# Optimization experiments

Hardware: AMD Instinct MI355X
Metric: run time of the kernel (lower is better)

## Reference

```python
import jax, jax.numpy as jnp
import numpy as np


def setup_inputs() -> dict:
    key = jax.random.key(0)
    k0, k1, k2 = jax.random.split(key, 3)
    B, S, E, U = 32, 2048, 512, 512
    return {
        "seq": jax.random.normal(k0, (B, S, E), jnp.float32),
        "w1": jax.random.normal(k1, (U, E), jnp.float32) * 0.05,
        "b1": jnp.zeros((U,), jnp.float32),
        "w2": jax.random.normal(k2, (3, U), jnp.float32) * 0.05,
        "b2": jnp.zeros((3,), jnp.float32),
        "num_lists": 16,
        "list_size": 16,
    }


def reference(seq, w1, b1, w2, b2, num_lists, list_size):
    B, S, E = seq.shape
    # action decoder: Linear -> SiLU -> Linear -> Softmax over 3 actions
    h = jax.nn.silu(jnp.einsum('bse,ue->bsu', seq, w1) + b1)
    actions = jax.nn.softmax(jnp.einsum('bsu,au->bsa', h, w2) + b2, axis=-1)  # (B,S,3)

    Hn, Wn = num_lists, list_size
    T0 = jnp.zeros((B, Hn, Wn), seq.dtype).at[:, 0, -1].set(1.0)   # superposition grid
    rs0 = jnp.zeros((B, Hn), seq.dtype).at[:, 0].set(1.0)          # row sums

    # process actions in reverse token order; scan over seq dim
    acts_rev = jnp.swapaxes(actions[:, ::-1, :], 0, 1)  # (S,B,3)

    def step(carry, a):
        T, rs = carry
        a0, a1, a2 = a[:, 0:1], a[:, 1:2], a[:, 2:3]  # each (B,1)
        # weight used to place the current (reversed) token: (a0+a1)*T
        w_step = (a0 + a1)[:, :, None] * T  # (B,H,W)
        # devolve: the grouped conv2d with kernel [0, a2, a0] is a width-shift blend
        other = a2[:, :, None] * T[:, :, :-1] + a0[:, :, None] * T[:, :, 1:]  # cols 0..W-2
        sums = a1 * jnp.roll(rs, 1, axis=1).at[:, 0].set(0.0)                 # (B,H)
        last = sums + a2 * T[:, :, -1]                                        # (B,H)
        rs_new = (a0 + a2) * rs + sums
        T_new = jnp.concatenate([other, last[:, :, None]], axis=2)
        return (T_new, rs_new), w_step

    _, ws = jax.lax.scan(step, (T0, rs0), acts_rev)  # ws: (S,B,H,W), aligned with reversed seq
    # G = sum_i w_i[...,None] * token_i[:,None,None,:]
    G = jnp.einsum('sbhw,bse->bhwe', ws, seq[:, ::-1, :])
    return G
```

## Files before the change

kernel.cpp:

```cpp
#include <hip/hip_runtime.h>
#include <stdint.h>

#define S_LEN 2048
#define NB 32
#define NE 512
#define NU 512
#define NP 256

typedef __bf16 bf16;
typedef __bf16 bf16x8 __attribute__((ext_vector_type(8)));
typedef __bf16 bf16x4 __attribute__((ext_vector_type(4)));
typedef float f32x4 __attribute__((ext_vector_type(4)));
typedef float f32x8 __attribute__((ext_vector_type(8)));

__device__ __forceinline__ void gload16(const void* g, void* l) {
    __builtin_amdgcn_global_load_lds(
        (__attribute__((address_space(1))) void*)g,
        (__attribute__((address_space(3))) void*)l, 16, 0, 0);
}

__device__ __forceinline__ float dpp_shr1_z(float x) {
    return __builtin_bit_cast(float, __builtin_amdgcn_update_dpp(
        0, __builtin_bit_cast(int, x), 0x111, 0xF, 0xF, true));
}
__device__ __forceinline__ float dpp_shl1_z(float x) {
    return __builtin_bit_cast(float, __builtin_amdgcn_update_dpp(
        0, __builtin_bit_cast(int, x), 0x101, 0xF, 0xF, true));
}

__device__ __forceinline__ void stage_tile(const bf16* __restrict__ src, int SR,
                                           bf16* lds, int tid) {
#pragma unroll
    for (int rnd = 0; rnd < 2; ++rnd) {
        const int c = rnd * 256 + tid;
        const int row = c >> 2;
        const int q = (c & 3) ^ ((c >> 3) & 3);
        gload16(src + (size_t)row * SR + q * 8, lds + c * 8);
    }
}

__global__ __launch_bounds__(256) void k_wconv(
    const float* __restrict__ w1, bf16* __restrict__ wHi, bf16* __restrict__ wLo)
{
    const int i = (blockIdx.x * 256 + threadIdx.x) * 4;
    const float4 v = *(const float4*)(w1 + i);
    const float vv[4] = {v.x, v.y, v.z, v.w};
    bf16x4 oh, ol;
#pragma unroll
    for (int q = 0; q < 4; ++q) {
        const bf16 hb = (bf16)vv[q];
        oh[q] = hb;
        ol[q] = (bf16)(vv[q] - (float)hb);
    }
    *(bf16x4*)(wHi + i) = oh;
    *(bf16x4*)(wLo + i) = ol;
}

__global__ __launch_bounds__(256, 2) void k_gemm1(
    const float* __restrict__ seq,
    const bf16* __restrict__ w1H, const bf16* __restrict__ w1L,
    const float* __restrict__ b1v, const float* __restrict__ w2,
    const float* __restrict__ b2v, float* __restrict__ actions)
{
    __shared__ __align__(16) bf16 BhL[2][4096];
    __shared__ __align__(16) bf16 BlL[2][4096];
    const int tid = threadIdx.x;
    const int wid = tid >> 6;
    const int lane = tid & 63;
    const int lr = lane & 15, lg = lane >> 4;
    const int m0 = blockIdx.x << 7;

    const float* arow0 = seq + (size_t)(m0 + wid * 32 + lr) * NE + lg * 8;
    const float* arow1 = arow0 + 16 * NE;
    const int lroff = lr * 64 + (lg ^ ((lr >> 1) & 3)) * 16;

    float plog[3][2][4];
#pragma unroll
    for (int a = 0; a < 3; ++a)
#pragma unroll
        for (int i = 0; i < 2; ++i)
#pragma unroll
            for (int q = 0; q < 4; ++q) plog[a][i][q] = 0.f;

    f32x4 acc[2][8];
    stage_tile(w1H, NE, BhL[0], tid);
    stage_tile(w1L, NE, BlL[0], tid);
    f32x8 Aa0 = *(const f32x8*)(arow0);
    f32x8 Aa1 = *(const f32x8*)(arow1);
    f32x8 Ab0, Ab1;

#define G1_BODY(g, buf, Ac0, Ac1, An0, An1) do {                              \
        __syncthreads();                                                      \
        if (((g) & 15) == 0) {                                                \
            _Pragma("unroll") for (int i = 0; i < 2; ++i)                     \
            _Pragma("unroll") for (int j = 0; j < 8; ++j)                     \
                acc[i][j] = (f32x4)(0.f);                                     \
        }                                                                     \
        bf16x8 bh[8], bl[8];                                                  \
        _Pragma("unroll") for (int j = 0; j < 8; ++j) {                       \
            bh[j] = *(const bf16x8*)((const char*)BhL[buf] + j * 1024 + lroff);\
            bl[j] = *(const bf16x8*)((const char*)BlL[buf] + j * 1024 + lroff);\
        }                                                                     \
        __syncthreads();                                                      \
        if ((g) < 63) {                                                       \
            const int gn = (g) + 1;                                           \
            const int u0n = (gn >> 4) << 7;                                   \
            const int k0n = (gn & 15) << 5;                                   \
            stage_tile(w1H + (size_t)u0n * NE + k0n, NE, BhL[(buf) ^ 1], tid);\
            stage_tile(w1L + (size_t)u0n * NE + k0n, NE, BlL[(buf) ^ 1], tid);\
            An0 = *(const f32x8*)(arow0 + k0n);                               \
            An1 = *(const f32x8*)(arow1 + k0n);                               \
        }                                                                     \
        bf16x8 Ah0, Al0, Ah1, Al1;                                            \
        _Pragma("unroll") for (int q = 0; q < 8; ++q) {                       \
            const bf16 h0 = (bf16)Ac0[q];                                     \
            Ah0[q] = h0; Al0[q] = (bf16)(Ac0[q] - (float)h0);                 \
            const bf16 h1 = (bf16)Ac1[q];                                     \
            Ah1[q] = h1; Al1[q] = (bf16)(Ac1[q] - (float)h1);                 \
        }                                                                     \
        _Pragma("unroll") for (int j = 0; j < 8; ++j) {                       \
            acc[0][j] = __builtin_amdgcn_mfma_f32_16x16x32_bf16(Ah0, bh[j], acc[0][j], 0, 0, 0); \
            acc[0][j] = __builtin_amdgcn_mfma_f32_16x16x32_bf16(Ah0, bl[j], acc[0][j], 0, 0, 0); \
            acc[0][j] = __builtin_amdgcn_mfma_f32_16x16x32_bf16(Al0, bh[j], acc[0][j], 0, 0, 0); \
            acc[1][j] = __builtin_amdgcn_mfma_f32_16x16x32_bf16(Ah1, bh[j], acc[1][j], 0, 0, 0); \
            acc[1][j] = __builtin_amdgcn_mfma_f32_16x16x32_bf16(Ah1, bl[j], acc[1][j], 0, 0, 0); \
            acc[1][j] = __builtin_amdgcn_mfma_f32_16x16x32_bf16(Al1, bh[j], acc[1][j], 0, 0, 0); \
        }                                                                     \
        if (((g) & 15) == 15) {                                               \
            const int u0 = ((g) >> 4) << 7;                                   \
            _Pragma("unroll") for (int j = 0; j < 8; ++j) {                   \
                const int col = u0 + j * 16 + lr;                             \
                const float b1c = b1v[col];                                   \
                const float w20 = w2[col], w21 = w2[NU + col], w22 = w2[2 * NU + col]; \
                _Pragma("unroll") for (int i = 0; i < 2; ++i)                 \
                _Pragma("unroll") for (int q = 0; q < 4; ++q) {               \
                    const float x = acc[i][j][q] + b1c;                       \
                    const float hgate = x / (1.f + __expf(-x));               \
                    plog[0][i][q] = fmaf(hgate, w20, plog[0][i][q]);          \
                    plog[1][i][q] = fmaf(hgate, w21, plog[1][i][q]);          \
                    plog[2][i][q] = fmaf(hgate, w22, plog[2][i][q]);          \
                }                                                             \
            }                                                                 \
        }                                                                     \
    } while (0)

    for (int gg = 0; gg < 32; ++gg) {
        G1_BODY(2 * gg, 0, Aa0, Aa1, Ab0, Ab1);
        G1_BODY(2 * gg + 1, 1, Ab0, Ab1, Aa0, Aa1);
    }
#undef G1_BODY

#pragma unroll
    for (int m = 1; m < 16; m <<= 1) {
#pragma unroll
        for (int a = 0; a < 3; ++a)
#pragma unroll
            for (int i = 0; i < 2; ++i)
#pragma unroll
                for (int q = 0; q < 4; ++q)
                    plog[a][i][q] += __shfl_xor(plog[a][i][q], m);
    }
    const float bb0 = b2v[0], bb1 = b2v[1], bb2 = b2v[2];
    if (lr == 0) {
#pragma unroll
        for (int i = 0; i < 2; ++i)
#pragma unroll
            for (int q = 0; q < 4; ++q) {
                const int row = m0 + wid * 32 + i * 16 + lg * 4 + q;
                const float l0 = plog[0][i][q] + bb0;
                const float l1 = plog[1][i][q] + bb1;
                const float l2 = plog[2][i][q] + bb2;
                const float mx = fmaxf(l0, fmaxf(l1, l2));
                const float e0 = __expf(l0 - mx), e1 = __expf(l1 - mx), e2 = __expf(l2 - mx);
                const float inv = 1.f / (e0 + e1 + e2);
                *(float4*)(actions + (size_t)row * 4) = make_float4(e0 * inv, e1 * inv, e2 * inv, 0.f);
            }
    }
}

union SPMem {
    float tile[64][65];
    struct {
        float4 actbuf[3][256];
        float  sums[2][256][16];
    } s;
};

__device__ __forceinline__ void rs_chunk(const float4* __restrict__ pb,
                                         float* __restrict__ so,
                                         float& rs, int lane)
{
    for (int w = 0; w < 32; ++w) {
        const int rtop = 255 - w * 8;
        const float4 e0 = pb[rtop],     e1 = pb[rtop - 1];
        const float4 e2 = pb[rtop - 2], e3 = pb[rtop - 3];
        const float4 e4 = pb[rtop - 4], e5 = pb[rtop - 5];
        const float4 e6 = pb[rtop - 6], e7 = pb[rtop - 7];
#define RS_STEP(E, k) do {                                                    \
        const float rsp = dpp_shr1_z(rs);                                     \
        const float s = (E).y * rsp;                                          \
        if (lane < 16) so[(rtop - (k)) * 16 + lane] = s;                      \
        rs = fmaf((E).x + (E).z, rs, s);                                      \
    } while (0)
        RS_STEP(e0, 0); RS_STEP(e1, 1); RS_STEP(e2, 2); RS_STEP(e3, 3);
        RS_STEP(e4, 4); RS_STEP(e5, 5); RS_STEP(e6, 6); RS_STEP(e7, 7);
#undef RS_STEP
    }
}

__device__ __forceinline__ void t_chunk(const float4* __restrict__ lb,
                                        const float* __restrict__ sp,
                                        float& T, bf16* __restrict__ obp,
                                        int tbase0, int w15)
{
    for (int w = 0; w < 32; ++w) {
        const int rtop = 255 - w * 8;
        const int tglob = tbase0 + rtop - 7;
        const float4 av0 = lb[rtop],     av1 = lb[rtop - 1];
        const float4 av2 = lb[rtop - 2], av3 = lb[rtop - 3];
        const float4 av4 = lb[rtop - 4], av5 = lb[rtop - 5];
        const float4 av6 = lb[rtop - 6], av7 = lb[rtop - 7];
        const float su0 = sp[rtop * 16],       su1 = sp[(rtop - 1) * 16];
        const float su2 = sp[(rtop - 2) * 16], su3 = sp[(rtop - 3) * 16];
        const float su4 = sp[(rtop - 4) * 16], su5 = sp[(rtop - 5) * 16];
        const float su6 = sp[(rtop - 6) * 16], su7 = sp[(rtop - 7) * 16];
        bf16x8 fr;
#define T_STEP(Av, Su, fi) do {                                               \
        const float a0 = (Av).x, a1 = (Av).y, a2 = (Av).z;                    \
        fr[fi] = (bf16)((a0 + a1) * T);                                       \
        const float nT = dpp_shl1_z(T);                                       \
        const float contrib = w15 ? (Su) : a0 * nT;                           \
        T = fmaf(a2, T, contrib);                                             \
    } while (0)
        T_STEP(av0, su0, 7); T_STEP(av1, su1, 6);
        T_STEP(av2, su2, 5); T_STEP(av3, su3, 4);
        T_STEP(av4, su4, 3); T_STEP(av5, su5, 2);
        T_STEP(av6, su6, 1); T_STEP(av7, su7, 0);
#undef T_STEP
        *(bf16x8*)(obp + tglob) = fr;
    }
}

__global__ __launch_bounds__(320) void k_scan_prep(
    const float* __restrict__ actions, bf16* __restrict__ wsT,
    const float* __restrict__ seq, bf16* __restrict__ tHi)
{
    __shared__ SPMem sm;
    const int tid = threadIdx.x;
    if (blockIdx.x < 32) {
        const int b = blockIdx.x;
        const int wid = tid >> 6;
        const int lane = tid & 63;
        const float4* actb = (const float4*)actions + (size_t)b * S_LEN;

        float rs = (lane == 0) ? 1.f : 0.f;
        float T = (wid == 0 && lane == 15) ? 1.f : 0.f;
        const int w15 = ((lane & 15) == 15) ? 1 : 0;
        bf16* obp = wsT + ((size_t)b * NP + wid * 64 + lane) * S_LEN;

        if (wid < 4) {
            gload16(actb + 1792 + wid * 64 + lane, &sm.s.actbuf[0][wid * 64]);
            gload16(actb + 1536 + wid * 64 + lane, &sm.s.actbuf[1][wid * 64]);
            asm volatile("s_waitcnt vmcnt(0)" ::: "memory");
        }
        __syncthreads();
        if (wid == 4) rs_chunk(sm.s.actbuf[0], &sm.s.sums[0][0][0], rs, lane);
        __syncthreads();

        int bufT = 0, bufP = 1, bufL = 2;
        for (int c = 0; c < 8; ++c) {
            if (wid < 4) {
                if (c < 6)
                    gload16(actb + (1280 - c * 256) + wid * 64 + lane,
                            &sm.s.actbuf[bufL][wid * 64]);
                t_chunk(sm.s.actbuf[bufT],
                        &sm.s.sums[c & 1][0][wid * 4 + (lane >> 4)],
                        T, obp, 1792 - c * 256, w15);
                asm volatile("s_waitcnt vmcnt(0)" ::: "memory");
            } else {
                if (c < 7)
                    rs_chunk(sm.s.actbuf[bufP], &sm.s.sums[(c + 1) & 1][0][0], rs, lane);
            }
            __syncthreads();
            const int t = bufT; bufT = bufP; bufP = bufL; bufL = t;
        }
        return;
    }
    const int bid = blockIdx.x - 32;
    const int b = bid >> 8;
    const int r = bid & 255;
    const int s0 = (r & 31) << 6;
    const int e0 = (r >> 5) << 6;
    const int tx = tid & 15, ty = (tid & 255) >> 4;
    const float* src = seq + ((size_t)b * S_LEN + s0) * NE + e0;
    if (tid < 256) {
#pragma unroll
        for (int i = 0; i < 4; ++i) {
            const int row = ty + i * 16;
            const float4 v = *(const float4*)(src + (size_t)row * NE + tx * 4);
            sm.tile[row][tx * 4 + 0] = v.x; sm.tile[row][tx * 4 + 1] = v.y;
            sm.tile[row][tx * 4 + 2] = v.z; sm.tile[row][tx * 4 + 3] = v.w;
        }
    }
    __syncthreads();
    if (tid < 256) {
        const int sx = tid & 7, ey = tid >> 3;
#pragma unroll
        for (int jj = 0; jj < 2; ++jj) {
            const int er = ey + jj * 32;
            bf16x8 oh;
#pragma unroll
            for (int q = 0; q < 8; ++q) oh[q] = (bf16)sm.tile[sx * 8 + q][er];
            *(bf16x8*)(tHi + ((size_t)b * NE + e0 + er) * S_LEN + s0 + sx * 8) = oh;
        }
    }
}

__global__ __launch_bounds__(256, 2) void k_gemm2(
    const bf16* __restrict__ wsT, const bf16* __restrict__ seqtH,
    float* __restrict__ part)
{
    __shared__ __align__(16) bf16 AL[2][4096];
    __shared__ __align__(16) bf16 BL[2][4096];
    const int tid = threadIdx.x;
    const int wid = tid >> 6;
    const int lane = tid & 63;
    const int lr = lane & 15, lg = lane >> 4;
    const int bid = blockIdx.x;
    const int b = bid >> 4;
    const int sub = bid & 15;
    const int kc = sub >> 3;
    const int p0 = ((sub >> 2) & 1) << 7;
    const int e0 = (sub & 3) << 7;

    const bf16* Abase = wsT + ((size_t)b * NP + p0) * S_LEN + kc * 1024;
    const bf16* Bbase = seqtH + ((size_t)b * NE + e0) * S_LEN + kc * 1024;
    const int lroff = lr * 64 + (lg ^ ((lr >> 1) & 3)) * 16;

    f32x4 acc[2][8];
#pragma unroll
    for (int i = 0; i < 2; ++i)
#pragma unroll
        for (int j = 0; j < 8; ++j) acc[i][j] = (f32x4)(0.f);

    stage_tile(Abase, S_LEN, AL[0], tid);
    stage_tile(Bbase, S_LEN, BL[0], tid);

#define G2_BODY(kt, buf) do {                                                 \
        __syncthreads();                                                      \
        bf16x8 af[2], bfv[8];                                                 \
        _Pragma("unroll") for (int i = 0; i < 2; ++i)                         \
            af[i] = *(const bf16x8*)((const char*)AL[buf]                     \
                     + (wid * 32 + i * 16) * 64 + lroff);                     \
        _Pragma("unroll") for (int j = 0; j < 8; ++j)                         \
            bfv[j] = *(const bf16x8*)((const char*)BL[buf] + j * 1024 + lroff);\
        __syncthreads();                                                      \
        if ((kt) < 31) {                                                      \
            stage_tile(Abase + ((kt) + 1) * 32, S_LEN, AL[(buf) ^ 1], tid);   \
            stage_tile(Bbase + ((kt) + 1) * 32, S_LEN, BL[(buf) ^ 1], tid);   \
        }                                                                     \
        _Pragma("unroll") for (int j = 0; j < 8; ++j) {                       \
            acc[0][j] = __builtin_amdgcn_mfma_f32_16x16x32_bf16(af[0], bfv[j], acc[0][j], 0, 0, 0); \
            acc[1][j] = __builtin_amdgcn_mfma_f32_16x16x32_bf16(af[1], bfv[j], acc[1][j], 0, 0, 0); \
        }                                                                     \
    } while (0)

    for (int kk = 0; kk < 16; ++kk) {
        G2_BODY(2 * kk, 0);
        G2_BODY(2 * kk + 1, 1);
    }
#undef G2_BODY

    float* obp = part + (((size_t)kc * NB + b) * NP + p0 + wid * 32) * NE + e0;
#pragma unroll
    for (int i = 0; i < 2; ++i)
#pragma unroll
        for (int j = 0; j < 8; ++j)
#pragma unroll
            for (int q = 0; q < 4; ++q)
                obp[(size_t)(i * 16 + lg * 4 + q) * NE + j * 16 + lr] = acc[i][j][q];
}

__global__ __launch_bounds__(256) void k_gred(
    const float* __restrict__ part, float* __restrict__ outp)
{
    const size_t i = ((size_t)blockIdx.x * 256 + threadIdx.x) * 4;
    const float4 p0 = *(const float4*)(part + i);
    const float4 p1 = *(const float4*)(part + ((size_t)NB * NP * NE) + i);
    *(float4*)(outp + i) = make_float4(p0.x + p1.x, p0.y + p1.y,
                                       p0.z + p1.z, p0.w + p1.w);
}

extern "C" void kernel_launch(void* const* d_in, const int* in_sizes, int n_in,
                              void* d_out, int out_size, void* d_ws, size_t ws_size,
                              hipStream_t stream) {
    (void)in_sizes; (void)n_in; (void)out_size; (void)ws_size;
    const float* seq = (const float*)d_in[0];
    const float* w1  = (const float*)d_in[1];
    const float* b1  = (const float*)d_in[2];
    const float* w2  = (const float*)d_in[3];
    const float* b2  = (const float*)d_in[4];
    float* outp = (float*)d_out;

    char* ws = (char*)d_ws;
    bf16*  seqtH   = (bf16*)(ws);
    bf16*  wsT     = (bf16*)(ws + (64ull << 20));
    float* actions = (float*)(ws + (96ull << 20));
    bf16*  w1H     = (bf16*)(ws + (97ull << 20));
    bf16*  w1L     = (bf16*)(ws + (97ull << 20) + (512u << 10));
    float* part    = (float*)(ws + (98ull << 20));

    hipLaunchKernelGGL(k_wconv, dim3(256),  dim3(256), 0, stream, w1, w1H, w1L);
    hipLaunchKernelGGL(k_gemm1, dim3(512),  dim3(256), 0, stream,
                       seq, w1H, w1L, b1, w2, b2, actions);
    hipLaunchKernelGGL(k_scan_prep, dim3(32 + 8192), dim3(320), 0, stream,
                       actions, wsT, seq, seqtH);
    hipLaunchKernelGGL(k_gemm2, dim3(512),  dim3(256), 0, stream, wsT, seqtH, part);
    hipLaunchKernelGGL(k_gred,  dim3(4096), dim3(256), 0, stream, part, outp);
}
```

Baseline: 289.4 us.

## Pre-split seq into bf16 hi/lo and halve gemm1 row tile for occupancy

Adds a separate kernel that converts seq into bf16 high and low parts once, so gemm1 loads pre-split bf16 operands instead of converting fp32 inside its main loop. gemm1 now handles 64 rows per block instead of 128, uses one accumulator set per wave, and targets 4 blocks per CU instead of 2. The cost is an extra full pass over seq (a read plus two bf16 writes) and more redundant staging of the w1 tiles, since twice as many blocks each load the same weights. The workspace layout is moved so the new buffers do not overlap existing ones.

```diff
diff --git a/kernel.cpp b/kernel.cpp
--- a/kernel.cpp
+++ b/kernel.cpp
@@ -39,6 +39,22 @@
     }
 }
 
+__global__ __launch_bounds__(256) void k_prep0(
+    const float* __restrict__ seq, bf16* __restrict__ sH, bf16* __restrict__ sL)
+{
+    const size_t i = ((size_t)blockIdx.x * 256 + threadIdx.x) * 8;
+    const f32x8 v = *(const f32x8*)(seq + i);
+    bf16x8 h, l;
+#pragma unroll
+    for (int q = 0; q < 8; ++q) {
+        const bf16 hb = (bf16)v[q];
+        h[q] = hb;
+        l[q] = (bf16)(v[q] - (float)hb);
+    }
+    *(bf16x8*)(sH + i) = h;
+    *(bf16x8*)(sL + i) = l;
+}
+
 __global__ __launch_bounds__(256) void k_wconv(
     const float* __restrict__ w1, bf16* __restrict__ wHi, bf16* __restrict__ wLo)
 {
@@ -56,8 +72,8 @@
     *(bf16x4*)(wLo + i) = ol;
 }
 
-__global__ __launch_bounds__(256, 2) void k_gemm1(
-    const float* __restrict__ seq,
+__global__ __launch_bounds__(256, 4) void k_gemm1(
+    const bf16* __restrict__ seqH, const bf16* __restrict__ seqL,
     const bf16* __restrict__ w1H, const bf16* __restrict__ w1L,
     const float* __restrict__ b1v, const float* __restrict__ w2,
     const float* __restrict__ b2v, float* __restrict__ actions)
@@ -68,33 +84,30 @@
     const int wid = tid >> 6;
     const int lane = tid & 63;
     const int lr = lane & 15, lg = lane >> 4;
-    const int m0 = blockIdx.x << 7;
-
-    const float* arow0 = seq + (size_t)(m0 + wid * 32 + lr) * NE + lg * 8;
-    const float* arow1 = arow0 + 16 * NE;
+    const int m0 = blockIdx.x << 6;
+
+    const bf16* ahp = seqH + (size_t)(m0 + wid * 16 + lr) * NE + lg * 8;
+    const bf16* alp = seqL + (size_t)(m0 + wid * 16 + lr) * NE + lg * 8;
     const int lroff = lr * 64 + (lg ^ ((lr >> 1) & 3)) * 16;
 
-    float plog[3][2][4];
+    float plog[3][4];
 #pragma unroll
     for (int a = 0; a < 3; ++a)
 #pragma unroll
-        for (int i = 0; i < 2; ++i)
-#pragma unroll
-            for (int q = 0; q < 4; ++q) plog[a][i][q] = 0.f;
-
-    f32x4 acc[2][8];
+        for (int q = 0; q < 4; ++q) plog[a][q] = 0.f;
+
+    f32x4 acc[8];
     stage_tile(w1H, NE, BhL[0], tid);
     stage_tile(w1L, NE, BlL[0], tid);
-    f32x8 Aa0 = *(const f32x8*)(arow0);
-    f32x8 Aa1 = *(const f32x8*)(arow1);
-    f32x8 Ab0, Ab1;
-
-#define G1_BODY(g, buf, Ac0, Ac1, An0, An1) do {                              \
+    bf16x8 AaH = *(const bf16x8*)(ahp);
+    bf16x8 AaL = *(const bf16x8*)(alp);
+    bf16x8 AbH, AbL;
+
+#define G1_BODY(g, buf, AcH, AcL, AnH, AnL) do {                              \
         __syncthreads();                                                      \
         if (((g) & 15) == 0) {                                                \
-            _Pragma("unroll") for (int i = 0; i < 2; ++i)                     \
             _Pragma("unroll") for (int j = 0; j < 8; ++j)                     \
-                acc[i][j] = (f32x4)(0.f);                                     \
+                acc[j] = (f32x4)(0.f);                                        \
         }                                                                     \
         bf16x8 bh[8], bl[8];                                                  \
         _Pragma("unroll") for (int j = 0; j < 8; ++j) {                       \
@@ -108,23 +121,13 @@
             const int k0n = (gn & 15) << 5;                                   \
             stage_tile(w1H + (size_t)u0n * NE + k0n, NE, BhL[(buf) ^ 1], tid);\
             stage_tile(w1L + (size_t)u0n * NE + k0n, NE, BlL[(buf) ^ 1], tid);\
-            An0 = *(const f32x8*)(arow0 + k0n);                               \
-            An1 = *(const f32x8*)(arow1 + k0n);                               \
-        }                                                                     \
-        bf16x8 Ah0, Al0, Ah1, Al1;                                            \
-        _Pragma("unroll") for (int q = 0; q < 8; ++q) {                       \
-            const bf16 h0 = (bf16)Ac0[q];                                     \
-            Ah0[q] = h0; Al0[q] = (bf16)(Ac0[q] - (float)h0);                 \
-            const bf16 h1 = (bf16)Ac1[q];                                     \
-            Ah1[q] = h1; Al1[q] = (bf16)(Ac1[q] - (float)h1);                 \
+            AnH = *(const bf16x8*)(ahp + k0n);                                \
+            AnL = *(const bf16x8*)(alp + k0n);                                \
         }                                                                     \
         _Pragma("unroll") for (int j = 0; j < 8; ++j) {                       \
-            acc[0][j] = __builtin_amdgcn_mfma_f32_16x16x32_bf16(Ah0, bh[j], acc[0][j], 0, 0, 0); \
-            acc[0][j] = __builtin_amdgcn_mfma_f32_16x16x32_bf16(Ah0, bl[j], acc[0][j], 0, 0, 0); \
-            acc[0][j] = __builtin_amdgcn_mfma_f32_16x16x32_bf16(Al0, bh[j], acc[0][j], 0, 0, 0); \
-            acc[1][j] = __builtin_amdgcn_mfma_f32_16x16x32_bf16(Ah1, bh[j], acc[1][j], 0, 0, 0); \
-            acc[1][j] = __builtin_amdgcn_mfma_f32_16x16x32_bf16(Ah1, bl[j], acc[1][j], 0, 0, 0); \
-            acc[1][j] = __builtin_amdgcn_mfma_f32_16x16x32_bf16(Al1, bh[j], acc[1][j], 0, 0, 0); \
+            acc[j] = __builtin_amdgcn_mfma_f32_16x16x32_bf16(AcH, bh[j], acc[j], 0, 0, 0); \
+            acc[j] = __builtin_amdgcn_mfma_f32_16x16x32_bf16(AcH, bl[j], acc[j], 0, 0, 0); \
+            acc[j] = __builtin_amdgcn_mfma_f32_16x16x32_bf16(AcL, bh[j], acc[j], 0, 0, 0); \
         }                                                                     \
         if (((g) & 15) == 15) {                                               \
             const int u0 = ((g) >> 4) << 7;                                   \
@@ -132,21 +135,20 @@
                 const int col = u0 + j * 16 + lr;                             \
                 const float b1c = b1v[col];                                   \
                 const float w20 = w2[col], w21 = w2[NU + col], w22 = w2[2 * NU + col]; \
-                _Pragma("unroll") for (int i = 0; i < 2; ++i)                 \
                 _Pragma("unroll") for (int q = 0; q < 4; ++q) {               \
-                    const float x = acc[i][j][q] + b1c;                       \
+                    const float x = acc[j][q] + b1c;                          \
                     const float hgate = x / (1.f + __expf(-x));               \
-                    plog[0][i][q] = fmaf(hgate, w20, plog[0][i][q]);          \
-                    plog[1][i][q] = fmaf(hgate, w21, plog[1][i][q]);          \
-                    plog[2][i][q] = fmaf(hgate, w22, plog[2][i][q]);          \
+                    plog[0][q] = fmaf(hgate, w20, plog[0][q]);                \
+                    plog[1][q] = fmaf(hgate, w21, plog[1][q]);                \
+                    plog[2][q] = fmaf(hgate, w22, plog[2][q]);                \
                 }                                                             \
             }                                                                 \
         }                                                                     \
     } while (0)
 
     for (int gg = 0; gg < 32; ++gg) {
-        G1_BODY(2 * gg, 0, Aa0, Aa1, Ab0, Ab1);
-        G1_BODY(2 * gg + 1, 1, Ab0, Ab1, Aa0, Aa1);
+        G1_BODY(2 * gg, 0, AaH, AaL, AbH, AbL);
+        G1_BODY(2 * gg + 1, 1, AbH, AbL, AaH, AaL);
     }
 #undef G1_BODY
 
@@ -155,26 +157,22 @@
 #pragma unroll
         for (int a = 0; a < 3; ++a)
 #pragma unroll
-            for (int i = 0; i < 2; ++i)
-#pragma unroll
-                for (int q = 0; q < 4; ++q)
-                    plog[a][i][q] += __shfl_xor(plog[a][i][q], m);
+            for (int q = 0; q < 4; ++q)
+                plog[a][q] += __shfl_xor(plog[a][q], m);
     }
     const float bb0 = b2v[0], bb1 = b2v[1], bb2 = b2v[2];
     if (lr == 0) {
 #pragma unroll
-        for (int i = 0; i < 2; ++i)
-#pragma unroll
-            for (int q = 0; q < 4; ++q) {
-                const int row = m0 + wid * 32 + i * 16 + lg * 4 + q;
-                const float l0 = plog[0][i][q] + bb0;
-                const float l1 = plog[1][i][q] + bb1;
-                const float l2 = plog[2][i][q] + bb2;
-                const float mx = fmaxf(l0, fmaxf(l1, l2));
-                const float e0 = __expf(l0 - mx), e1 = __expf(l1 - mx), e2 = __expf(l2 - mx);
-                const float inv = 1.f / (e0 + e1 + e2);
-                *(float4*)(actions + (size_t)row * 4) = make_float4(e0 * inv, e1 * inv, e2 * inv, 0.f);
-            }
+        for (int q = 0; q < 4; ++q) {
+            const int row = m0 + wid * 16 + lg * 4 + q;
+            const float l0 = plog[0][q] + bb0;
+            const float l1 = plog[1][q] + bb1;
+            const float l2 = plog[2][q] + bb2;
+            const float mx = fmaxf(l0, fmaxf(l1, l2));
+            const float e0 = __expf(l0 - mx), e1 = __expf(l1 - mx), e2 = __expf(l2 - mx);
+            const float inv = 1.f / (e0 + e1 + e2);
+            *(float4*)(actions + (size_t)row * 4) = make_float4(e0 * inv, e1 * inv, e2 * inv, 0.f);
+        }
     }
 }
 
@@ -403,16 +401,19 @@
     float* outp = (float*)d_out;
 
     char* ws = (char*)d_ws;
+    bf16*  seqH    = (bf16*)(ws);
     bf16*  seqtH   = (bf16*)(ws);
+    bf16*  seqL    = (bf16*)(ws + (64ull << 20));
     bf16*  wsT     = (bf16*)(ws + (64ull << 20));
-    float* actions = (float*)(ws + (96ull << 20));
-    bf16*  w1H     = (bf16*)(ws + (97ull << 20));
-    bf16*  w1L     = (bf16*)(ws + (97ull << 20) + (512u << 10));
-    float* part    = (float*)(ws + (98ull << 20));
-
-    hipLaunchKernelGGL(k_wconv, dim3(256),  dim3(256), 0, stream, w1, w1H, w1L);
-    hipLaunchKernelGGL(k_gemm1, dim3(512),  dim3(256), 0, stream,
-                       seq, w1H, w1L, b1, w2, b2, actions);
+    float* part    = (float*)(ws + (128ull << 20));
+    float* actions = (float*)(ws + (160ull << 20));
+    bf16*  w1H     = (bf16*)(ws + (161ull << 20));
+    bf16*  w1L     = (bf16*)(ws + (161ull << 20) + (512u << 10));
+
+    hipLaunchKernelGGL(k_wconv, dim3(256),   dim3(256), 0, stream, w1, w1H, w1L);
+    hipLaunchKernelGGL(k_prep0, dim3(16384), dim3(256), 0, stream, seq, seqH, seqL);
+    hipLaunchKernelGGL(k_gemm1, dim3(1024),  dim3(256), 0, stream,
+                       seqH, seqL, w1H, w1L, b1, w2, b2, actions);
     hipLaunchKernelGGL(k_scan_prep, dim3(32 + 8192), dim3(320), 0, stream,
                        actions, wsT, seq, seqtH);
     hipLaunchKernelGGL(k_gemm2, dim3(512),  dim3(256), 0, stream, wsT, seqtH, part);
```

After: 428.3 us. 1.48x slower.

## Restructure gemm1 into 8-wave 2x4 warp tiling with 256-wide U tiles

Applied to the files above, without the earlier changes.

The first GEMM block grows from 4 to 8 waves. Waves are arranged as 2 along M and 4 along U, and each wave computes a 64x64 sub-tile over 256-column U panels instead of a 32x128 strip. This halves the number of K-step iterations and cuts redundant reloads of the A rows, which are converted to split-bf16, because each wave now reuses 4 A fragments across 4 B fragments. The per-row logits are now produced by four waves each, so an added LDS cross-wave reduction combines them before the softmax. The cost is larger LDS buffers and more registers per thread, which may reduce occupancy.

```diff
diff --git a/kernel.cpp b/kernel.cpp
--- a/kernel.cpp
+++ b/kernel.cpp
@@ -56,97 +56,108 @@
     *(bf16x4*)(wLo + i) = ol;
 }
 
-__global__ __launch_bounds__(256, 2) void k_gemm1(
+__device__ __forceinline__ void g1_stage(const bf16* __restrict__ w1H,
+                                         const bf16* __restrict__ w1L,
+                                         int g, bf16* dH, bf16* dL, int tid) {
+#pragma unroll
+    for (int rnd = 0; rnd < 2; ++rnd) {
+        const int c = rnd * 512 + tid;
+        const int row = c >> 2;
+        const int q = (c & 3) ^ ((c >> 3) & 3);
+        const size_t so = (size_t)((g >> 4) * 256 + row) * NE + (g & 15) * 32 + q * 8;
+        gload16(w1H + so, dH + c * 8);
+        gload16(w1L + so, dL + c * 8);
+    }
+}
+
+__global__ __launch_bounds__(512, 2) void k_gemm1(
     const float* __restrict__ seq,
     const bf16* __restrict__ w1H, const bf16* __restrict__ w1L,
     const float* __restrict__ b1v, const float* __restrict__ w2,
     const float* __restrict__ b2v, float* __restrict__ actions)
 {
-    __shared__ __align__(16) bf16 BhL[2][4096];
-    __shared__ __align__(16) bf16 BlL[2][4096];
+    __shared__ __align__(16) bf16 BhL[2][8192];
+    __shared__ __align__(16) bf16 BlL[2][8192];
+    __shared__ float red[4][2][4][4][4][3];
     const int tid = threadIdx.x;
     const int wid = tid >> 6;
+    const int wm = wid >> 2, wu = wid & 3;
     const int lane = tid & 63;
     const int lr = lane & 15, lg = lane >> 4;
     const int m0 = blockIdx.x << 7;
 
-    const float* arow0 = seq + (size_t)(m0 + wid * 32 + lr) * NE + lg * 8;
-    const float* arow1 = arow0 + 16 * NE;
-    const int lroff = lr * 64 + (lg ^ ((lr >> 1) & 3)) * 16;
-
-    float plog[3][2][4];
+    const float* ar[4];
+#pragma unroll
+    for (int i = 0; i < 4; ++i)
+        ar[i] = seq + (size_t)(m0 + wm * 64 + i * 16 + lr) * NE + lg * 8;
+    const int lbase = (wu * 64 + lr) * 64 + (lg ^ ((lr >> 1) & 3)) * 16;
+
+    float plog[3][4][4];
 #pragma unroll
     for (int a = 0; a < 3; ++a)
 #pragma unroll
-        for (int i = 0; i < 2; ++i)
+        for (int i = 0; i < 4; ++i)
 #pragma unroll
             for (int q = 0; q < 4; ++q) plog[a][i][q] = 0.f;
 
-    f32x4 acc[2][8];
-    stage_tile(w1H, NE, BhL[0], tid);
-    stage_tile(w1L, NE, BlL[0], tid);
-    f32x8 Aa0 = *(const f32x8*)(arow0);
-    f32x8 Aa1 = *(const f32x8*)(arow1);
-    f32x8 Ab0, Ab1;
-
-#define G1_BODY(g, buf, Ac0, Ac1, An0, An1) do {                              \
+    f32x4 acc[4][4];
+    g1_stage(w1H, w1L, 0, BhL[0], BlL[0], tid);
+    f32x8 AC[4], AN[4];
+#pragma unroll
+    for (int i = 0; i < 4; ++i) AC[i] = *(const f32x8*)(ar[i]);
+
+#define G1_BODY(g, buf, Ac, An) do {                                          \
         __syncthreads();                                                      \
         if (((g) & 15) == 0) {                                                \
-            _Pragma("unroll") for (int i = 0; i < 2; ++i)                     \
-            _Pragma("unroll") for (int j = 0; j < 8; ++j)                     \
+            _Pragma("unroll") for (int i = 0; i < 4; ++i)                     \
+            _Pragma("unroll") for (int j = 0; j < 4; ++j)                     \
                 acc[i][j] = (f32x4)(0.f);                                     \
         }                                                                     \
-        bf16x8 bh[8], bl[8];                                                  \
-        _Pragma("unroll") for (int j = 0; j < 8; ++j) {                       \
-            bh[j] = *(const bf16x8*)((const char*)BhL[buf] + j * 1024 + lroff);\
-            bl[j] = *(const bf16x8*)((const char*)BlL[buf] + j * 1024 + lroff);\
+        bf16x8 bh[4], bl[4];                                                  \
+        _Pragma("unroll") for (int j = 0; j < 4; ++j) {                       \
+            bh[j] = *(const bf16x8*)((const char*)BhL[buf] + j * 1024 + lbase);\
+            bl[j] = *(const bf16x8*)((const char*)BlL[buf] + j * 1024 + lbase);\
         }                                                                     \
         __syncthreads();                                                      \
-        if ((g) < 63) {                                                       \
-            const int gn = (g) + 1;                                           \
-            const int u0n = (gn >> 4) << 7;                                   \
-            const int k0n = (gn & 15) << 5;                                   \
-            stage_tile(w1H + (size_t)u0n * NE + k0n, NE, BhL[(buf) ^ 1], tid);\
-            stage_tile(w1L + (size_t)u0n * NE + k0n, NE, BlL[(buf) ^ 1], tid);\
-            An0 = *(const f32x8*)(arow0 + k0n);                               \
-            An1 = *(const f32x8*)(arow1 + k0n);                               \
-        }                                                                     \
-        bf16x8 Ah0, Al0, Ah1, Al1;                                            \
-        _Pragma("unroll") for (int q = 0; q < 8; ++q) {                       \
-            const bf16 h0 = (bf16)Ac0[q];                                     \
-            Ah0[q] = h0; Al0[q] = (bf16)(Ac0[q] - (float)h0);                 \
-            const bf16 h1 = (bf16)Ac1[q];                                     \
-            Ah1[q] = h1; Al1[q] = (bf16)(Ac1[q] - (float)h1);                 \
-        }                                                                     \
-        _Pragma("unroll") for (int j = 0; j < 8; ++j) {                       \
-            acc[0][j] = __builtin_amdgcn_mfma_f32_16x16x32_bf16(Ah0, bh[j], acc[0][j], 0, 0, 0); \
-            acc[0][j] = __builtin_amdgcn_mfma_f32_16x16x32_bf16(Ah0, bl[j], acc[0][j], 0, 0, 0); \
-            acc[0][j] = __builtin_amdgcn_mfma_f32_16x16x32_bf16(Al0, bh[j], acc[0][j], 0, 0, 0); \
-            acc[1][j] = __builtin_amdgcn_mfma_f32_16x16x32_bf16(Ah1, bh[j], acc[1][j], 0, 0, 0); \
-            acc[1][j] = __builtin_amdgcn_mfma_f32_16x16x32_bf16(Ah1, bl[j], acc[1][j], 0, 0, 0); \
-            acc[1][j] = __builtin_amdgcn_mfma_f32_16x16x32_bf16(Al1, bh[j], acc[1][j], 0, 0, 0); \
+        if ((g) < 31) {                                                       \
+            g1_stage(w1H, w1L, (g) + 1, BhL[(buf) ^ 1], BlL[(buf) ^ 1], tid); \
+            const int ktn = ((g) + 1) & 15;                                   \
+            _Pragma("unroll") for (int i = 0; i < 4; ++i)                     \
+                An[i] = *(const f32x8*)(ar[i] + ktn * 32);                    \
+        }                                                                     \
+        bf16x8 Ah[4], Al[4];                                                  \
+        _Pragma("unroll") for (int i = 0; i < 4; ++i)                         \
+        _Pragma("unroll") for (int e = 0; e < 8; ++e) {                       \
+            const bf16 hb = (bf16)Ac[i][e];                                   \
+            Ah[i][e] = hb; Al[i][e] = (bf16)(Ac[i][e] - (float)hb);           \
+        }                                                                     \
+        _Pragma("unroll") for (int j = 0; j < 4; ++j)                         \
+        _Pragma("unroll") for (int i = 0; i < 4; ++i) {                       \
+            acc[i][j] = __builtin_amdgcn_mfma_f32_16x16x32_bf16(Ah[i], bh[j], acc[i][j], 0, 0, 0); \
+            acc[i][j] = __builtin_amdgcn_mfma_f32_16x16x32_bf16(Ah[i], bl[j], acc[i][j], 0, 0, 0); \
+            acc[i][j] = __builtin_amdgcn_mfma_f32_16x16x32_bf16(Al[i], bh[j], acc[i][j], 0, 0, 0); \
         }                                                                     \
         if (((g) & 15) == 15) {                                               \
-            const int u0 = ((g) >> 4) << 7;                                   \
-            _Pragma("unroll") for (int j = 0; j < 8; ++j) {                   \
-                const int col = u0 + j * 16 + lr;                             \
+            const int p = (g) >> 4;                                           \
+            _Pragma("unroll") for (int j = 0; j < 4; ++j) {                   \
+                const int col = p * 256 + wu * 64 + j * 16 + lr;              \
                 const float b1c = b1v[col];                                   \
                 const float w20 = w2[col], w21 = w2[NU + col], w22 = w2[2 * NU + col]; \
-                _Pragma("unroll") for (int i = 0; i < 2; ++i)                 \
+                _Pragma("unroll") for (int i = 0; i < 4; ++i)                 \
                 _Pragma("unroll") for (int q = 0; q < 4; ++q) {               \
                     const float x = acc[i][j][q] + b1c;                       \
-                    const float hgate = x / (1.f + __expf(-x));               \
-                    plog[0][i][q] = fmaf(hgate, w20, plog[0][i][q]);          \
-                    plog[1][i][q] = fmaf(hgate, w21, plog[1][i][q]);          \
-                    plog[2][i][q] = fmaf(hgate, w22, plog[2][i][q]);          \
+                    const float hg = x / (1.f + __expf(-x));                  \
+                    plog[0][i][q] = fmaf(hg, w20, plog[0][i][q]);             \
+                    plog[1][i][q] = fmaf(hg, w21, plog[1][i][q]);             \
+                    plog[2][i][q] = fmaf(hg, w22, plog[2][i][q]);             \
                 }                                                             \
             }                                                                 \
         }                                                                     \
     } while (0)
 
-    for (int gg = 0; gg < 32; ++gg) {
-        G1_BODY(2 * gg, 0, Aa0, Aa1, Ab0, Ab1);
-        G1_BODY(2 * gg + 1, 1, Ab0, Ab1, Aa0, Aa1);
+    for (int gg = 0; gg < 16; ++gg) {
+        G1_BODY(2 * gg, 0, AC, AN);
+        G1_BODY(2 * gg + 1, 1, AN, AC);
     }
 #undef G1_BODY
 
@@ -155,26 +166,35 @@
 #pragma unroll
         for (int a = 0; a < 3; ++a)
 #pragma unroll
-            for (int i = 0; i < 2; ++i)
+            for (int i = 0; i < 4; ++i)
 #pragma unroll
                 for (int q = 0; q < 4; ++q)
                     plog[a][i][q] += __shfl_xor(plog[a][i][q], m);
     }
-    const float bb0 = b2v[0], bb1 = b2v[1], bb2 = b2v[2];
     if (lr == 0) {
 #pragma unroll
-        for (int i = 0; i < 2; ++i)
-#pragma unroll
-            for (int q = 0; q < 4; ++q) {
-                const int row = m0 + wid * 32 + i * 16 + lg * 4 + q;
-                const float l0 = plog[0][i][q] + bb0;
-                const float l1 = plog[1][i][q] + bb1;
-                const float l2 = plog[2][i][q] + bb2;
-                const float mx = fmaxf(l0, fmaxf(l1, l2));
-                const float e0 = __expf(l0 - mx), e1 = __expf(l1 - mx), e2 = __expf(l2 - mx);
-                const float inv = 1.f / (e0 + e1 + e2);
-                *(float4*)(actions + (size_t)row * 4) = make_float4(e0 * inv, e1 * inv, e2 * inv, 0.f);
-            }
+        for (int a = 0; a < 3; ++a)
+#pragma unroll
+            for (int i = 0; i < 4; ++i)
+#pragma unroll
+            for (int q = 0; q < 4; ++q)
+                red[wu][wm][i][lg][q][a] = plog[a][i][q];
+    }
+    __syncthreads();
+    if (tid < 128) {
+        const int r = tid;
+        const int wmr = r >> 6, ir = (r >> 4) & 3, lgr = (r >> 2) & 3, qr = r & 3;
+        float l0 = b2v[0], l1 = b2v[1], l2 = b2v[2];
+#pragma unroll
+        for (int u = 0; u < 4; ++u) {
+            l0 += red[u][wmr][ir][lgr][qr][0];
+            l1 += red[u][wmr][ir][lgr][qr][1];
+            l2 += red[u][wmr][ir][lgr][qr][2];
+        }
+        const float mx = fmaxf(l0, fmaxf(l1, l2));
+        const float e0 = __expf(l0 - mx), e1 = __expf(l1 - mx), e2 = __expf(l2 - mx);
+        const float inv = 1.f / (e0 + e1 + e2);
+        *(float4*)(actions + (size_t)(m0 + r) * 4) = make_float4(e0 * inv, e1 * inv, e2 * inv, 0.f);
     }
 }
 
@@ -411,7 +431,7 @@
     float* part    = (float*)(ws + (98ull << 20));
 
     hipLaunchKernelGGL(k_wconv, dim3(256),  dim3(256), 0, stream, w1, w1H, w1L);
-    hipLaunchKernelGGL(k_gemm1, dim3(512),  dim3(256), 0, stream,
+    hipLaunchKernelGGL(k_gemm1, dim3(512),  dim3(512), 0, stream,
                        seq, w1H, w1L, b1, w2, b2, actions);
     hipLaunchKernelGGL(k_scan_prep, dim3(32 + 8192), dim3(320), 0, stream,
                        actions, wsT, seq, seqtH);
```

Result: slower. 380.2 us (+31.4%).
